# Optimization experiments

Hardware: AMD Instinct MI355X
Metric: run time of the kernel (lower is better)

Reference implementation:

```python
import jax, jax.numpy as jnp
import numpy as np

N_CTX = 4096
D_MODEL = 1024
D_HEAD = 64


def setup_inputs() -> dict:
    key = jax.random.key(0)
    k_x, k_q, k_k, k_o, k_v = jax.random.split(key, 5)
    return {
        "x": jax.random.normal(k_x, (N_CTX, D_MODEL), dtype=jnp.float32),
        "W_q": jax.random.normal(k_q, (D_MODEL, D_HEAD), dtype=jnp.float32),
        "W_kT": jax.random.normal(k_k, (D_HEAD, D_MODEL), dtype=jnp.float32),
        "W_o": jax.random.normal(k_o, (D_MODEL, D_HEAD), dtype=jnp.float32),
        "W_vT": jax.random.normal(k_v, (D_HEAD, D_MODEL), dtype=jnp.float32),
    }


def reference(x, W_q, W_kT, W_o, W_vT):
    # x: [n, d_model]
    n = x.shape[0]
    q = x @ W_q                      # [n, d_head]
    k = x @ W_kT.T                   # [n, d_head]  (W_kT @ x.T transposed)
    scores = q @ k.T                 # [n, n] -- NOTE: original has no 1/sqrt(d_head) scaling
    # causal mask: upper triangle (strictly above diagonal) set to -inf
    causal = jnp.tril(jnp.ones((n, n), dtype=bool))
    scores = jnp.where(causal, scores, -jnp.inf)
    attn = jax.nn.softmax(scores, axis=1)  # softmax over keys (dim=1)
    v = x @ W_o @ W_vT               # [n, d_model] -- faithful to attn @ x @ W_o @ W_vT
    return attn @ v                  # [n, d_model]
```

## Files before the change

### kernel.cpp

```cpp
#include <hip/hip_runtime.h>
#include <hip/hip_bf16.h>
#include <math.h>

#define DM    1024
#define DH    64
#define NCTX  4096
#define NCH   8

typedef __attribute__((ext_vector_type(8))) _Float16 f16x8;
typedef __attribute__((ext_vector_type(4))) float f32x4;

#define D_QH   0
#define D_QM   524288
#define D_KH   1572864
#define D_KM   2097152
#define D_UTB  3145728
#define D_PY   3670016
#define D_PM   12058624
#define D_PL   12189696
#define D_WTH  12320768
#define D_WTM  12713984

#define S_WVH  0
#define S_WVM  131072
#define S_PM   262144
#define S_PL   393216
#define S_PY   524288
#define S_END  8912896
#define S_YH   262144
#define S_YM   786432

__device__ __forceinline__ ushort f2h(float x) {
  _Float16 h = (_Float16)x;
  return __builtin_bit_cast(ushort, h);
}
__device__ __forceinline__ float h2f(ushort u) {
  return (float)__builtin_bit_cast(_Float16, u);
}

typedef __attribute__((address_space(1))) const unsigned int gas_u32;
typedef __attribute__((address_space(3))) unsigned int las_u32;
__device__ __forceinline__ void gload_lds16(const void* g, void* l) {
  __builtin_amdgcn_global_load_lds((gas_u32*)g, (las_u32*)l, 16, 0, 0);
}

__global__ __launch_bounds__(256) void wsplit_kernel(
    const float* __restrict__ Wq, const float* __restrict__ WkT,
    const float* __restrict__ Wo, const float* __restrict__ Wv,
    ushort* __restrict__ WTh, ushort* __restrict__ WTm,
    ushort* __restrict__ WvTh, ushort* __restrict__ WvTm)
{
  int gid = blockIdx.x * 256 + threadIdx.x;
  int mat = gid >> 16;
  int idx = gid & 65535;
  if (mat == 3) {
    float v = Wv[idx];
    int h = idx >> 10, c = idx & 1023;
    int oidx = c * 64 + h;
    ushort h16 = f2h(v);
    WvTh[oidx] = h16;
    WvTm[oidx] = f2h(v - h2f(h16));
    return;
  }
  float v; int oidx;
  if (mat == 1) {
    v = WkT[idx];
    oidx = 65536 + idx;
  } else {
    int k = idx >> 6, h = idx & 63;
    v = (mat == 0 ? Wq : Wo)[idx];
    oidx = mat * 65536 + h * 1024 + k;
  }
  ushort h16 = f2h(v);
  float rem = v - h2f(h16);
  WTh[oidx] = h16;
  WTm[oidx] = f2h(rem);
}

__global__ __launch_bounds__(256, 2) void proj_mfma_kernel(
    const float* __restrict__ x,
    const ushort* __restrict__ WTh, const ushort* __restrict__ WTm,
    ushort* __restrict__ Qh, ushort* __restrict__ Qm,
    ushort* __restrict__ Kh, ushort* __restrict__ Km,
    ushort* __restrict__ UTb)
{
  __shared__ __align__(16) ushort xsh[32*128], xsm[32*128];
  __shared__ __align__(16) ushort wsh[2][64*128], wsm[2][64*128];

  const int tid  = threadIdx.x;
  const int lane = tid & 63;
  const int w    = tid >> 6;
  const int q16  = lane & 15;
  const int grp  = lane >> 4;
  const int r0   = blockIdx.x * 32;
  const int mat  = blockIdx.y;
  const ushort* __restrict__ wh = WTh + mat * 65536;
  const ushort* __restrict__ wm = WTm + mat * 65536;

  const int rw  = (w & 1) * 16;
  const int ct0 = (w >> 1) * 2;

  const int xrowl = tid >> 4, xslot = tid & 15;

  auto stage_w = [&](int b, int s) {
    const int kp0 = s * 128;
    #pragma unroll
    for (int u = 0; u < 4; ++u) {
      int ubase = u * 256 + w * 64;
      int unit  = ubase + lane;
      int row   = unit >> 4, slotp = unit & 15;
      int ssrc  = slotp ^ (row & 15);
      int gsrc  = row * DM + kp0 + ssrc * 8;
      gload_lds16(&wh[gsrc], &wsh[b][ubase * 8]);
      gload_lds16(&wm[gsrc], &wsm[b][ubase * 8]);
    }
  };
  auto xload = [&](int s, float4& a0, float4& a1, float4& b0, float4& b1) {
    const int kp0 = s * 128;
    const float* s0 = &x[(r0 + xrowl) * DM + kp0 + xslot * 8];
    const float* s1 = &x[(r0 + xrowl + 16) * DM + kp0 + xslot * 8];
    a0 = *(const float4*)&s0[0]; a1 = *(const float4*)&s0[4];
    b0 = *(const float4*)&s1[0]; b1 = *(const float4*)&s1[4];
  };
  auto xsplit_write = [&](float4 a0, float4 a1, float4 b0, float4 b1) {
    float xv0[8] = {a0.x,a0.y,a0.z,a0.w,a1.x,a1.y,a1.z,a1.w};
    float xv1[8] = {b0.x,b0.y,b0.z,b0.w,b1.x,b1.y,b1.z,b1.w};
    ushort hv0[8], mv0[8], hv1[8], mv1[8];
    #pragma unroll
    for (int e = 0; e < 8; ++e) {
      ushort h0 = f2h(xv0[e]);
      hv0[e] = h0;  mv0[e] = f2h(xv0[e] - h2f(h0));
      ushort h1 = f2h(xv1[e]);
      hv1[e] = h1;  mv1[e] = f2h(xv1[e] - h2f(h1));
    }
    int d0 = xrowl * 128 + ((xslot ^ (xrowl & 15)) << 3);
    int r1 = xrowl + 16;
    int d1 = r1 * 128 + ((xslot ^ (r1 & 15)) << 3);
    #pragma unroll
    for (int e = 0; e < 8; ++e) {
      xsh[d0+e] = hv0[e]; xsm[d0+e] = mv0[e];
      xsh[d1+e] = hv1[e]; xsm[d1+e] = mv1[e];
    }
  };

  f32x4 acc[2] = {{0,0,0,0},{0,0,0,0}};

  {
    float4 a0, a1, b0, b1;
    xload(0, a0, a1, b0, b1);
    xsplit_write(a0, a1, b0, b1);
    stage_w(0, 0);
  }
  __syncthreads();

  int cur = 0;
  for (int stg = 0; stg < 8; ++stg) {
    float4 na0, na1, nb0, nb1;
    if (stg < 7) {
      xload(stg + 1, na0, na1, nb0, nb1);
      stage_w(cur ^ 1, stg + 1);
    }
    #pragma unroll
    for (int ksub = 0; ksub < 4; ++ksub) {
      const int s = ksub * 4 + grp;
      const int xrow = rw + q16;
      f16x8 xh8 = *(const f16x8*)&xsh[xrow * 128 + ((s ^ (xrow & 15)) << 3)];
      f16x8 xm8 = *(const f16x8*)&xsm[xrow * 128 + ((s ^ (xrow & 15)) << 3)];
      #pragma unroll
      for (int i = 0; i < 2; ++i) {
        const int wrow = (ct0 + i) * 16 + q16;
        const int woff = wrow * 128 + ((s ^ (wrow & 15)) << 3);
        f16x8 bh = *(const f16x8*)&wsh[cur][woff];
        f16x8 bm = *(const f16x8*)&wsm[cur][woff];
        if (mat == 2) {
          acc[i] = __builtin_amdgcn_mfma_f32_16x16x32_f16(bh, xh8, acc[i], 0,0,0);
          acc[i] = __builtin_amdgcn_mfma_f32_16x16x32_f16(bh, xm8, acc[i], 0,0,0);
          acc[i] = __builtin_amdgcn_mfma_f32_16x16x32_f16(bm, xh8, acc[i], 0,0,0);
        } else {
          acc[i] = __builtin_amdgcn_mfma_f32_16x16x32_f16(xh8, bh, acc[i], 0,0,0);
          acc[i] = __builtin_amdgcn_mfma_f32_16x16x32_f16(xh8, bm, acc[i], 0,0,0);
          acc[i] = __builtin_amdgcn_mfma_f32_16x16x32_f16(xm8, bh, acc[i], 0,0,0);
        }
      }
    }
    __syncthreads();
    if (stg < 7) xsplit_write(na0, na1, nb0, nb1);
    __syncthreads();
    cur ^= 1;
  }

  if (mat == 2) {
    #pragma unroll
    for (int i = 0; i < 2; ++i)
      #pragma unroll
      for (int r = 0; r < 4; ++r)
        UTb[((ct0 + i)*16 + 4*grp + r) * NCTX + r0 + rw + q16] = f2h(acc[i][r]);
  } else {
    ushort* __restrict__ Dh = (mat == 0) ? Qh : Kh;
    ushort* __restrict__ Dm = (mat == 0) ? Qm : Km;
    #pragma unroll
    for (int i = 0; i < 2; ++i)
      #pragma unroll
      for (int r = 0; r < 4; ++r) {
        float v = acc[i][r];
        ushort h = f2h(v);
        ushort m = f2h(v - h2f(h));
        int idx = (r0 + rw + 4*grp + r) * DH + (ct0 + i)*16 + q16;
        Dh[idx] = h; Dm[idx] = m;
      }
  }
}

__global__ __launch_bounds__(256, 2) void attn_kernel(
    const ushort* __restrict__ Qh, const ushort* __restrict__ Qm,
    const ushort* __restrict__ Kh, const ushort* __restrict__ Km,
    const ushort* __restrict__ UTb,
    float* __restrict__ Pm, float* __restrict__ Pl, float* __restrict__ Py)
{
  __shared__ ushort Ksh[2][2][64*64];
  __shared__ ushort Ush[2][64*64];
  __shared__ __align__(16) ushort ps[4][16*72];

  const int tid  = threadIdx.x;
  const int lane = tid & 63;
  const int w    = tid >> 6;
  ushort* psw = ps[w];
  const int q16  = lane & 15;
  const int grp  = lane >> 4;
  const int colb = grp * 8;

  const int qq    = blockIdx.x;
  const int c     = blockIdx.y;
  const int gbase = 252 - 4 * qq;
  const int g     = gbase + w;
  const int gmax  = gbase + 3;
  const int T     = ((16*gmax + 15) >> 6) + 1;
  const int t0 = (c * T) >> 3, t1 = ((c+1) * T) >> 3;
  const int Town = ((16*g + 15) >> 6) + 1;
  const int q0 = 16 * g;
  const int q  = q0 + q16;

  auto stage = [&](int b, int t) {
    const int j0 = t * 64;
    #pragma unroll
    for (int it = 0; it < 2; ++it) {
      int ubase = it * 256 + w * 64;
      int unit  = ubase + lane;
      int row   = unit >> 3, slotp = unit & 7;
      int c8    = slotp ^ (row & 7);
      int src   = (j0 + row) * DH + c8 * 8;
      gload_lds16(&Kh[src], &Ksh[b][0][ubase * 8]);
      gload_lds16(&Km[src], &Ksh[b][1][ubase * 8]);
      gload_lds16(&UTb[row * NCTX + j0 + c8 * 8], &Ush[b][ubase * 8]);
    }
  };

  f16x8 fqh[2], fqm[2];
  #pragma unroll
  for (int ks = 0; ks < 2; ++ks) {
    int off = (q0 + q16)*DH + 32*ks + colb;
    fqh[ks] = *(const f16x8*)&Qh[off];
    fqm[ks] = *(const f16x8*)&Qm[off];
  }

  float mrun = -3.0e38f, lrun = 0.f;
  f32x4 yacc[4] = {{0,0,0,0},{0,0,0,0},{0,0,0,0},{0,0,0,0}};

  if (t0 < t1) stage(0, t0);
  __syncthreads();

  int cur = 0;
  for (int t = t0; t < t1; ++t) {
    if (t + 1 < t1) stage(cur ^ 1, t + 1);
    if (t < Town) {
      const int j0 = t * 64;
      f32x4 sa[4] = {{0,0,0,0},{0,0,0,0},{0,0,0,0},{0,0,0,0}};
      #pragma unroll
      for (int ks = 0; ks < 2; ++ks) {
        #pragma unroll
        for (int st = 0; st < 4; ++st) {
          int row = 16*st + q16;
          int off = row * 64 + (((4*ks + grp) ^ (row & 7)) << 3);
          f16x8 kh = *(const f16x8*)&Ksh[cur][0][off];
          f16x8 km = *(const f16x8*)&Ksh[cur][1][off];
          sa[st] = __builtin_amdgcn_mfma_f32_16x16x32_f16(kh, fqh[ks], sa[st], 0,0,0);
          sa[st] = __builtin_amdgcn_mfma_f32_16x16x32_f16(kh, fqm[ks], sa[st], 0,0,0);
          sa[st] = __builtin_amdgcn_mfma_f32_16x16x32_f16(km, fqh[ks], sa[st], 0,0,0);
        }
      }
      #pragma unroll
      for (int st = 0; st < 4; ++st)
        #pragma unroll
        for (int r = 0; r < 4; ++r) {
          int key = j0 + 16*st + 4*grp + r;
          if (key > q) sa[st][r] = -3.0e38f;
        }
      float mx = sa[0][0];
      #pragma unroll
      for (int st = 0; st < 4; ++st)
        #pragma unroll
        for (int r = 0; r < 4; ++r) mx = fmaxf(mx, sa[st][r]);
      mx = fmaxf(mx, __shfl_xor(mx, 16));
      mx = fmaxf(mx, __shfl_xor(mx, 32));
      float mnew  = fmaxf(mrun, mx);
      float alpha = __expf(mrun - mnew);
      float ts = 0.f;
      ushort pb[16];
      #pragma unroll
      for (int st = 0; st < 4; ++st)
        #pragma unroll
        for (int r = 0; r < 4; ++r) {
          float p = __expf(sa[st][r] - mnew);
          ts += p;
          pb[st*4 + r] = f2h(p);
        }
      ts += __shfl_xor(ts, 16);
      ts += __shfl_xor(ts, 32);
      lrun = lrun * alpha + ts;
      mrun = mnew;
      float ar[4];
      #pragma unroll
      for (int r = 0; r < 4; ++r) ar[r] = __shfl(alpha, 4*grp + r, 64);
      #pragma unroll
      for (int dt = 0; dt < 4; ++dt) {
        yacc[dt][0] *= ar[0]; yacc[dt][1] *= ar[1];
        yacc[dt][2] *= ar[2]; yacc[dt][3] *= ar[3];
      }
      #pragma unroll
      for (int st = 0; st < 4; ++st) {
        uint2 v;
        v.x = (uint)pb[st*4+0] | ((uint)pb[st*4+1] << 16);
        v.y = (uint)pb[st*4+2] | ((uint)pb[st*4+3] << 16);
        *(uint2*)&psw[q16*72 + 16*st + 4*grp] = v;
      }
      __threadfence_block();
      __builtin_amdgcn_sched_barrier(0);
      #pragma unroll
      for (int ks = 0; ks < 2; ++ks) {
        f16x8 pa = *(const f16x8*)&psw[q16*72 + 32*ks + colb];
        #pragma unroll
        for (int dt = 0; dt < 4; ++dt) {
          int row = 16*dt + q16;
          int off = row * 64 + (((4*ks + grp) ^ (row & 7)) << 3);
          f16x8 ub = *(const f16x8*)&Ush[cur][off];
          yacc[dt] = __builtin_amdgcn_mfma_f32_16x16x32_f16(pa, ub, yacc[dt], 0,0,0);
        }
      }
    }
    __syncthreads();
    cur ^= 1;
  }
  if (grp == 0) {
    Pm[c * NCTX + q] = mrun;
    Pl[c * NCTX + q] = lrun;
  }
  #pragma unroll
  for (int dt = 0; dt < 4; ++dt)
    #pragma unroll
    for (int r = 0; r < 4; ++r)
      Py[(c * NCTX + q0 + 4*grp + r) * DH + 16*dt + q16] = yacc[dt][r];
}

__global__ __launch_bounds__(256, 3) void out_fused_kernel(
    const float* __restrict__ Pm, const float* __restrict__ Pl,
    const float* __restrict__ Py,
    const ushort* __restrict__ WvTh, const ushort* __restrict__ WvTm,
    float* __restrict__ out)
{
  __shared__ __align__(16) ushort Yh[64*64], Ym[64*64];
  __shared__ __align__(16) ushort Wsh[128*64], Wsm[128*64];
  __shared__ float sden[NCH][64];
  __shared__ float invd[64];

  const int tid  = threadIdx.x;
  const int lane = tid & 63;
  const int w    = tid >> 6;
  const int q16  = lane & 15;
  const int grp  = lane >> 4;
  const int r0   = blockIdx.x * 64;
  const int cb   = blockIdx.y;

  #pragma unroll
  for (int u = 0; u < 4; ++u) {
    int ubase = u * 256 + w * 64;
    int unit  = ubase + lane;
    int row   = unit >> 3, slotp = unit & 7;
    int c8    = slotp ^ (row & 7);
    int src   = (cb * 128 + row) * 64 + c8 * 8;
    gload_lds16(&WvTh[src], &Wsh[ubase * 8]);
    gload_lds16(&WvTm[src], &Wsm[ubase * 8]);
  }
  if (tid < 64) {
    int rrow = r0 + tid;
    float mv[NCH]; float M = -3.0e38f;
    #pragma unroll
    for (int c = 0; c < NCH; ++c) {
      mv[c] = Pm[c*NCTX + rrow];
      M = fmaxf(M, mv[c]);
    }
    float den = 0.f;
    #pragma unroll
    for (int c = 0; c < NCH; ++c) {
      float s = __expf(mv[c] - M);
      sden[c][tid] = s;
      den += s * Pl[c*NCTX + rrow];
    }
    invd[tid] = 1.0f / den;
  }
  __syncthreads();

  #pragma unroll
  for (int it = 0; it < 4; ++it) {
    int idx = it * 256 + tid;
    int h4 = idx & 15, rr = idx >> 4;
    int rrow = r0 + rr;
    float nx = 0.f, ny = 0.f, nz = 0.f, nw = 0.f;
    #pragma unroll
    for (int c = 0; c < NCH; ++c) {
      float s = sden[c][rr];
      float4 p4 = *(const float4*)&Py[(c*NCTX + rrow)*DH + h4*4];
      nx += s*p4.x; ny += s*p4.y; nz += s*p4.z; nw += s*p4.w;
    }
    float inv = invd[rr];
    float yv[4] = {nx*inv, ny*inv, nz*inv, nw*inv};
    ushort hv[4], mv4[4];
    #pragma unroll
    for (int e = 0; e < 4; ++e) {
      ushort h = f2h(yv[e]);
      hv[e] = h;
      mv4[e] = f2h(yv[e] - h2f(h));
    }
    int off = rr*64 + (((h4 >> 1) ^ (rr & 7)) << 3) + (h4 & 1) * 4;
    uint2 vh, vm;
    vh.x = (uint)hv[0] | ((uint)hv[1] << 16);
    vh.y = (uint)hv[2] | ((uint)hv[3] << 16);
    vm.x = (uint)mv4[0] | ((uint)mv4[1] << 16);
    vm.y = (uint)mv4[2] | ((uint)mv4[3] << 16);
    *(uint2*)&Yh[off] = vh;
    *(uint2*)&Ym[off] = vm;
  }
  __syncthreads();

  f32x4 acc[4][2] = {};
  #pragma unroll
  for (int ks = 0; ks < 2; ++ks) {
    f16x8 ah[4], am[4];
    #pragma unroll
    for (int rt = 0; rt < 4; ++rt) {
      int row = 16*rt + q16;
      int off = row*64 + (((4*ks + grp) ^ (row & 7)) << 3);
      ah[rt] = *(const f16x8*)&Yh[off];
      am[rt] = *(const f16x8*)&Ym[off];
    }
    #pragma unroll
    for (int lt = 0; lt < 2; ++lt) {
      int crow = w*32 + lt*16 + q16;
      int off  = crow*64 + (((4*ks + grp) ^ (crow & 7)) << 3);
      f16x8 bh = *(const f16x8*)&Wsh[off];
      f16x8 bm = *(const f16x8*)&Wsm[off];
      #pragma unroll
      for (int rt = 0; rt < 4; ++rt) {
        acc[rt][lt] = __builtin_amdgcn_mfma_f32_16x16x32_f16(ah[rt], bh, acc[rt][lt], 0,0,0);
        acc[rt][lt] = __builtin_amdgcn_mfma_f32_16x16x32_f16(ah[rt], bm, acc[rt][lt], 0,0,0);
        acc[rt][lt] = __builtin_amdgcn_mfma_f32_16x16x32_f16(am[rt], bh, acc[rt][lt], 0,0,0);
      }
    }
  }
  #pragma unroll
  for (int rt = 0; rt < 4; ++rt)
    #pragma unroll
    for (int lt = 0; lt < 2; ++lt)
      #pragma unroll
      for (int r = 0; r < 4; ++r)
        out[(r0 + 16*rt + 4*grp + r) * DM + cb*128 + w*32 + lt*16 + q16] = acc[rt][lt][r];
}

__global__ __launch_bounds__(256) void combine_kernel(
    const float* __restrict__ Pm, const float* __restrict__ Pl,
    const float* __restrict__ Py,
    ushort* __restrict__ Yh, ushort* __restrict__ Ym)
{
  int idx = blockIdx.x * 256 + threadIdx.x;
  int r = idx >> 6, d = idx & 63;
  float mv[NCH];
  float M = -3.0e38f;
  #pragma unroll
  for (int c = 0; c < NCH; ++c) {
    mv[c] = Pm[c*NCTX + r];
    M = fmaxf(M, mv[c]);
  }
  float num = 0.f, den = 0.f;
  #pragma unroll
  for (int c = 0; c < NCH; ++c) {
    float s = __expf(mv[c] - M);
    den += s * Pl[c*NCTX + r];
    num += s * Py[(c*NCTX + r)*DH + d];
  }
  float y = num / den;
  ushort h = f2h(y);
  Yh[idx] = h;
  Ym[idx] = f2h(y - h2f(h));
}

__global__ __launch_bounds__(256, 3) void out_mfma_kernel(
    const ushort* __restrict__ Yh_g, const ushort* __restrict__ Ym_g,
    const ushort* __restrict__ WvTh, const ushort* __restrict__ WvTm,
    float* __restrict__ out)
{
  __shared__ __align__(16) ushort Yh[64*64], Ym[64*64];
  __shared__ __align__(16) ushort Wsh[128*64], Wsm[128*64];

  const int tid  = threadIdx.x;
  const int lane = tid & 63;
  const int w    = tid >> 6;
  const int q16  = lane & 15;
  const int grp  = lane >> 4;
  const int r0   = blockIdx.x * 64;
  const int cb   = blockIdx.y;

  #pragma unroll
  for (int it = 0; it < 2; ++it) {
    int ubase = it * 256 + w * 64;
    int unit  = ubase + lane;
    int row   = unit >> 3, slotp = unit & 7;
    int c8    = slotp ^ (row & 7);
    int src   = (r0 + row) * 64 + c8 * 8;
    gload_lds16(&Yh_g[src], &Yh[ubase * 8]);
    gload_lds16(&Ym_g[src], &Ym[ubase * 8]);
  }
  #pragma unroll
  for (int u = 0; u < 4; ++u) {
    int ubase = u * 256 + w * 64;
    int unit  = ubase + lane;
    int row   = unit >> 3, slotp = unit & 7;
    int c8    = slotp ^ (row & 7);
    int src   = (cb * 128 + row) * 64 + c8 * 8;
    gload_lds16(&WvTh[src], &Wsh[ubase * 8]);
    gload_lds16(&WvTm[src], &Wsm[ubase * 8]);
  }
  __syncthreads();

  f32x4 acc[4][2] = {};
  #pragma unroll
  for (int ks = 0; ks < 2; ++ks) {
    f16x8 ah[4], am[4];
    #pragma unroll
    for (int rt = 0; rt < 4; ++rt) {
      int row = 16*rt + q16;
      int off = row*64 + (((4*ks + grp) ^ (row & 7)) << 3);
      ah[rt] = *(const f16x8*)&Yh[off];
      am[rt] = *(const f16x8*)&Ym[off];
    }
    #pragma unroll
    for (int lt = 0; lt < 2; ++lt) {
      int crow = w*32 + lt*16 + q16;
      int off  = crow*64 + (((4*ks + grp) ^ (crow & 7)) << 3);
      f16x8 bh = *(const f16x8*)&Wsh[off];
      f16x8 bm = *(const f16x8*)&Wsm[off];
      #pragma unroll
      for (int rt = 0; rt < 4; ++rt) {
        acc[rt][lt] = __builtin_amdgcn_mfma_f32_16x16x32_f16(ah[rt], bh, acc[rt][lt], 0,0,0);
        acc[rt][lt] = __builtin_amdgcn_mfma_f32_16x16x32_f16(ah[rt], bm, acc[rt][lt], 0,0,0);
        acc[rt][lt] = __builtin_amdgcn_mfma_f32_16x16x32_f16(am[rt], bh, acc[rt][lt], 0,0,0);
      }
    }
  }
  #pragma unroll
  for (int rt = 0; rt < 4; ++rt)
    #pragma unroll
    for (int lt = 0; lt < 2; ++lt)
      #pragma unroll
      for (int r = 0; r < 4; ++r)
        out[(r0 + 16*rt + 4*grp + r) * DM + cb*128 + w*32 + lt*16 + q16] = acc[rt][lt][r];
}

extern "C" void kernel_launch(void* const* d_in, const int* in_sizes, int n_in,
                              void* d_out, int out_size, void* d_ws, size_t ws_size,
                              hipStream_t stream) {
  const float* x   = (const float*)d_in[0];
  const float* Wq  = (const float*)d_in[1];
  const float* WkT = (const float*)d_in[2];
  const float* Wo  = (const float*)d_in[3];
  const float* Wv  = (const float*)d_in[4];
  float* out = (float*)d_out;
  char*  ob  = (char*)d_out;
  char*  wb  = (char*)d_ws;

  ushort* Qhp = (ushort*)(ob + D_QH);
  ushort* Qmp = (ushort*)(ob + D_QM);
  ushort* Khp = (ushort*)(ob + D_KH);
  ushort* Kmp = (ushort*)(ob + D_KM);
  ushort* UTb = (ushort*)(ob + D_UTB);
  ushort* WTh = (ushort*)(ob + D_WTH);
  ushort* WTm = (ushort*)(ob + D_WTM);

  ushort* WvTh = (ushort*)(wb + S_WVH);
  ushort* WvTm = (ushort*)(wb + S_WVM);

  const bool big_ws = (ws_size >= (size_t)S_END);

  float* Pmp = big_ws ? (float*)(wb + S_PM) : (float*)(ob + D_PM);
  float* Plp = big_ws ? (float*)(wb + S_PL) : (float*)(ob + D_PL);
  float* Pyp = big_ws ? (float*)(wb + S_PY) : (float*)(ob + D_PY);

  hipLaunchKernelGGL(wsplit_kernel, dim3(1024), dim3(256), 0, stream,
                     Wq, WkT, Wo, Wv, WTh, WTm, WvTh, WvTm);
  hipLaunchKernelGGL(proj_mfma_kernel, dim3(128, 3), dim3(256), 0, stream,
                     x, WTh, WTm, Qhp, Qmp, Khp, Kmp, UTb);
  hipLaunchKernelGGL(attn_kernel, dim3(64, 8), dim3(256), 0, stream,
                     Qhp, Qmp, Khp, Kmp, UTb, Pmp, Plp, Pyp);
  if (big_ws) {
    hipLaunchKernelGGL(out_fused_kernel, dim3(64, 8), dim3(256), 0, stream,
                       Pmp, Plp, Pyp, WvTh, WvTm, out);
  } else {
    ushort* Yhp = (ushort*)(wb + S_YH);
    ushort* Ymp = (ushort*)(wb + S_YM);
    hipLaunchKernelGGL(combine_kernel, dim3(1024), dim3(256), 0, stream,
                       Pmp, Plp, Pyp, Yhp, Ymp);
    hipLaunchKernelGGL(out_mfma_kernel, dim3(64, 8), dim3(256), 0, stream,
                       Yhp, Ymp, WvTh, WvTm, out);
  }
}
```

Measured before the change: 55.08 us.

## Fuse split-KV combine and output projection into attention via last-block counter

The separate out_fused kernel is removed. Its combine-and-project epilogue now runs inside attn_kernel: an atomic counter per query tile elects the last of the 8 KV-chunk blocks, which merges the partial softmax states and multiplies by W_vT across all 8 column blocks. This also moves intermediates into the workspace under a larger workspace threshold, and adds a memset to clear the counters. The intent is to save a kernel launch and its tail. The cost is that one block per query tile serially does eight output tiles' worth of work, which can lengthen the critical path. It also relies on the workspace being large enough for the new layout, and otherwise falls back to the old multi-kernel path.

```diff
diff --git a/kernel.cpp b/kernel.cpp
--- a/kernel.cpp
+++ b/kernel.cpp
@@ -9,6 +9,21 @@
 
 typedef __attribute__((ext_vector_type(8))) _Float16 f16x8;
 typedef __attribute__((ext_vector_type(4))) float f32x4;
+
+#define P_WVH  0
+#define P_WVM  131072
+#define P_CNT  262144
+#define P_WTH  266240
+#define P_WTM  659456
+#define P_QH   1052672
+#define P_QM   1576960
+#define P_KH   2101248
+#define P_KM   2625536
+#define P_UTB  3149824
+#define P_PM   3674112
+#define P_PL   3805184
+#define P_PY   3936256
+#define P_END  12324864
 
 #define D_QH   0
 #define D_QM   524288
@@ -20,13 +35,8 @@
 #define D_PL   12189696
 #define D_WTH  12320768
 #define D_WTM  12713984
-
 #define S_WVH  0
 #define S_WVM  131072
-#define S_PM   262144
-#define S_PL   393216
-#define S_PY   524288
-#define S_END  8912896
 #define S_YH   262144
 #define S_YM   786432
 
@@ -211,20 +221,35 @@
   }
 }
 
+union SmemU {
+  struct {
+    ushort Ksh[2][2][64*64];
+    ushort Ush[2][64*64];
+    ushort ps[4][16*72];
+  } a;
+  struct {
+    ushort Yh[64*64], Ym[64*64];
+    ushort Wsh[128*64], Wsm[128*64];
+    float  sden[NCH][64];
+    float  invd[64];
+  } f;
+};
+
 __global__ __launch_bounds__(256, 2) void attn_kernel(
     const ushort* __restrict__ Qh, const ushort* __restrict__ Qm,
     const ushort* __restrict__ Kh, const ushort* __restrict__ Km,
     const ushort* __restrict__ UTb,
-    float* __restrict__ Pm, float* __restrict__ Pl, float* __restrict__ Py)
+    float* __restrict__ Pm, float* __restrict__ Pl, float* __restrict__ Py,
+    const ushort* __restrict__ WvTh, const ushort* __restrict__ WvTm,
+    float* __restrict__ out, int* __restrict__ cnt, int do_fin)
 {
-  __shared__ ushort Ksh[2][2][64*64];
-  __shared__ ushort Ush[2][64*64];
-  __shared__ __align__(16) ushort ps[4][16*72];
+  __shared__ __align__(16) SmemU sm;
+  __shared__ int fin;
 
   const int tid  = threadIdx.x;
   const int lane = tid & 63;
   const int w    = tid >> 6;
-  ushort* psw = ps[w];
+  ushort* psw = sm.a.ps[w];
   const int q16  = lane & 15;
   const int grp  = lane >> 4;
   const int colb = grp * 8;
@@ -249,9 +274,9 @@
       int row   = unit >> 3, slotp = unit & 7;
       int c8    = slotp ^ (row & 7);
       int src   = (j0 + row) * DH + c8 * 8;
-      gload_lds16(&Kh[src], &Ksh[b][0][ubase * 8]);
-      gload_lds16(&Km[src], &Ksh[b][1][ubase * 8]);
-      gload_lds16(&UTb[row * NCTX + j0 + c8 * 8], &Ush[b][ubase * 8]);
+      gload_lds16(&Kh[src], &sm.a.Ksh[b][0][ubase * 8]);
+      gload_lds16(&Km[src], &sm.a.Ksh[b][1][ubase * 8]);
+      gload_lds16(&UTb[row * NCTX + j0 + c8 * 8], &sm.a.Ush[b][ubase * 8]);
     }
   };
 
@@ -281,8 +306,8 @@
         for (int st = 0; st < 4; ++st) {
           int row = 16*st + q16;
           int off = row * 64 + (((4*ks + grp) ^ (row & 7)) << 3);
-          f16x8 kh = *(const f16x8*)&Ksh[cur][0][off];
-          f16x8 km = *(const f16x8*)&Ksh[cur][1][off];
+          f16x8 kh = *(const f16x8*)&sm.a.Ksh[cur][0][off];
+          f16x8 km = *(const f16x8*)&sm.a.Ksh[cur][1][off];
           sa[st] = __builtin_amdgcn_mfma_f32_16x16x32_f16(kh, fqh[ks], sa[st], 0,0,0);
           sa[st] = __builtin_amdgcn_mfma_f32_16x16x32_f16(kh, fqm[ks], sa[st], 0,0,0);
           sa[st] = __builtin_amdgcn_mfma_f32_16x16x32_f16(km, fqh[ks], sa[st], 0,0,0);
@@ -342,7 +367,7 @@
         for (int dt = 0; dt < 4; ++dt) {
           int row = 16*dt + q16;
           int off = row * 64 + (((4*ks + grp) ^ (row & 7)) << 3);
-          f16x8 ub = *(const f16x8*)&Ush[cur][off];
+          f16x8 ub = *(const f16x8*)&sm.a.Ush[cur][off];
           yacc[dt] = __builtin_amdgcn_mfma_f32_16x16x32_f16(pa, ub, yacc[dt], 0,0,0);
         }
       }
@@ -359,53 +384,37 @@
     #pragma unroll
     for (int r = 0; r < 4; ++r)
       Py[(c * NCTX + q0 + 4*grp + r) * DH + 16*dt + q16] = yacc[dt][r];
-}
-
-__global__ __launch_bounds__(256, 3) void out_fused_kernel(
-    const float* __restrict__ Pm, const float* __restrict__ Pl,
-    const float* __restrict__ Py,
-    const ushort* __restrict__ WvTh, const ushort* __restrict__ WvTm,
-    float* __restrict__ out)
-{
-  __shared__ __align__(16) ushort Yh[64*64], Ym[64*64];
-  __shared__ __align__(16) ushort Wsh[128*64], Wsm[128*64];
-  __shared__ float sden[NCH][64];
-  __shared__ float invd[64];
-
-  const int tid  = threadIdx.x;
-  const int lane = tid & 63;
-  const int w    = tid >> 6;
-  const int q16  = lane & 15;
-  const int grp  = lane >> 4;
-  const int r0   = blockIdx.x * 64;
-  const int cb   = blockIdx.y;
-
-  #pragma unroll
-  for (int u = 0; u < 4; ++u) {
-    int ubase = u * 256 + w * 64;
-    int unit  = ubase + lane;
-    int row   = unit >> 3, slotp = unit & 7;
-    int c8    = slotp ^ (row & 7);
-    int src   = (cb * 128 + row) * 64 + c8 * 8;
-    gload_lds16(&WvTh[src], &Wsh[ubase * 8]);
-    gload_lds16(&WvTm[src], &Wsm[ubase * 8]);
-  }
+
+  if (!do_fin) return;
+
+  __threadfence();
+  __syncthreads();
+  if (tid == 0) {
+    int old = atomicAdd(&cnt[qq], 1);
+    fin = (old == 7);
+  }
+  __syncthreads();
+  if (!fin) return;
+  __threadfence();
+
+  const int rq0 = 16 * gbase;
+
   if (tid < 64) {
-    int rrow = r0 + tid;
+    int rrow = rq0 + tid;
     float mv[NCH]; float M = -3.0e38f;
     #pragma unroll
-    for (int c = 0; c < NCH; ++c) {
-      mv[c] = Pm[c*NCTX + rrow];
-      M = fmaxf(M, mv[c]);
+    for (int cc = 0; cc < NCH; ++cc) {
+      mv[cc] = Pm[cc*NCTX + rrow];
+      M = fmaxf(M, mv[cc]);
     }
     float den = 0.f;
     #pragma unroll
-    for (int c = 0; c < NCH; ++c) {
-      float s = __expf(mv[c] - M);
-      sden[c][tid] = s;
-      den += s * Pl[c*NCTX + rrow];
-    }
-    invd[tid] = 1.0f / den;
+    for (int cc = 0; cc < NCH; ++cc) {
+      float s = __expf(mv[cc] - M);
+      sm.f.sden[cc][tid] = s;
+      den += s * Pl[cc*NCTX + rrow];
+    }
+    sm.f.invd[tid] = 1.0f / den;
   }
   __syncthreads();
 
@@ -413,15 +422,15 @@
   for (int it = 0; it < 4; ++it) {
     int idx = it * 256 + tid;
     int h4 = idx & 15, rr = idx >> 4;
-    int rrow = r0 + rr;
+    int rrow = rq0 + rr;
     float nx = 0.f, ny = 0.f, nz = 0.f, nw = 0.f;
     #pragma unroll
-    for (int c = 0; c < NCH; ++c) {
-      float s = sden[c][rr];
-      float4 p4 = *(const float4*)&Py[(c*NCTX + rrow)*DH + h4*4];
+    for (int cc = 0; cc < NCH; ++cc) {
+      float s = sm.f.sden[cc][rr];
+      float4 p4 = *(const float4*)&Py[(cc*NCTX + rrow)*DH + h4*4];
       nx += s*p4.x; ny += s*p4.y; nz += s*p4.z; nw += s*p4.w;
     }
-    float inv = invd[rr];
+    float inv = sm.f.invd[rr];
     float yv[4] = {nx*inv, ny*inv, nz*inv, nw*inv};
     ushort hv[4], mv4[4];
     #pragma unroll
@@ -436,43 +445,57 @@
     vh.y = (uint)hv[2] | ((uint)hv[3] << 16);
     vm.x = (uint)mv4[0] | ((uint)mv4[1] << 16);
     vm.y = (uint)mv4[2] | ((uint)mv4[3] << 16);
-    *(uint2*)&Yh[off] = vh;
-    *(uint2*)&Ym[off] = vm;
-  }
-  __syncthreads();
-
-  f32x4 acc[4][2] = {};
-  #pragma unroll
-  for (int ks = 0; ks < 2; ++ks) {
-    f16x8 ah[4], am[4];
-    #pragma unroll
-    for (int rt = 0; rt < 4; ++rt) {
-      int row = 16*rt + q16;
-      int off = row*64 + (((4*ks + grp) ^ (row & 7)) << 3);
-      ah[rt] = *(const f16x8*)&Yh[off];
-      am[rt] = *(const f16x8*)&Ym[off];
-    }
-    #pragma unroll
-    for (int lt = 0; lt < 2; ++lt) {
-      int crow = w*32 + lt*16 + q16;
-      int off  = crow*64 + (((4*ks + grp) ^ (crow & 7)) << 3);
-      f16x8 bh = *(const f16x8*)&Wsh[off];
-      f16x8 bm = *(const f16x8*)&Wsm[off];
+    *(uint2*)&sm.f.Yh[off] = vh;
+    *(uint2*)&sm.f.Ym[off] = vm;
+  }
+
+  for (int cb2 = 0; cb2 < 8; ++cb2) {
+    __syncthreads();
+    #pragma unroll
+    for (int u = 0; u < 4; ++u) {
+      int ubase = u * 256 + w * 64;
+      int unit  = ubase + lane;
+      int row   = unit >> 3, slotp = unit & 7;
+      int c8    = slotp ^ (row & 7);
+      int src   = (cb2 * 128 + row) * 64 + c8 * 8;
+      gload_lds16(&WvTh[src], &sm.f.Wsh[ubase * 8]);
+      gload_lds16(&WvTm[src], &sm.f.Wsm[ubase * 8]);
+    }
+    __syncthreads();
+
+    f32x4 acc[4][2] = {};
+    #pragma unroll
+    for (int ks = 0; ks < 2; ++ks) {
+      f16x8 ah[4], am[4];
       #pragma unroll
       for (int rt = 0; rt < 4; ++rt) {
-        acc[rt][lt] = __builtin_amdgcn_mfma_f32_16x16x32_f16(ah[rt], bh, acc[rt][lt], 0,0,0);
-        acc[rt][lt] = __builtin_amdgcn_mfma_f32_16x16x32_f16(ah[rt], bm, acc[rt][lt], 0,0,0);
-        acc[rt][lt] = __builtin_amdgcn_mfma_f32_16x16x32_f16(am[rt], bh, acc[rt][lt], 0,0,0);
-      }
-    }
-  }
-  #pragma unroll
-  for (int rt = 0; rt < 4; ++rt)
-    #pragma unroll
-    for (int lt = 0; lt < 2; ++lt)
-      #pragma unroll
-      for (int r = 0; r < 4; ++r)
-        out[(r0 + 16*rt + 4*grp + r) * DM + cb*128 + w*32 + lt*16 + q16] = acc[rt][lt][r];
+        int row = 16*rt + q16;
+        int off = row*64 + (((4*ks + grp) ^ (row & 7)) << 3);
+        ah[rt] = *(const f16x8*)&sm.f.Yh[off];
+        am[rt] = *(const f16x8*)&sm.f.Ym[off];
+      }
+      #pragma unroll
+      for (int lt = 0; lt < 2; ++lt) {
+        int crow = w*32 + lt*16 + q16;
+        int off  = crow*64 + (((4*ks + grp) ^ (crow & 7)) << 3);
+        f16x8 bh = *(const f16x8*)&sm.f.Wsh[off];
+        f16x8 bm = *(const f16x8*)&sm.f.Wsm[off];
+        #pragma unroll
+        for (int rt = 0; rt < 4; ++rt) {
+          acc[rt][lt] = __builtin_amdgcn_mfma_f32_16x16x32_f16(ah[rt], bh, acc[rt][lt], 0,0,0);
+          acc[rt][lt] = __builtin_amdgcn_mfma_f32_16x16x32_f16(ah[rt], bm, acc[rt][lt], 0,0,0);
+          acc[rt][lt] = __builtin_amdgcn_mfma_f32_16x16x32_f16(am[rt], bh, acc[rt][lt], 0,0,0);
+        }
+      }
+    }
+    #pragma unroll
+    for (int rt = 0; rt < 4; ++rt)
+      #pragma unroll
+      for (int lt = 0; lt < 2; ++lt)
+        #pragma unroll
+        for (int r = 0; r < 4; ++r)
+          out[(rq0 + 16*rt + 4*grp + r) * DM + cb2*128 + w*32 + lt*16 + q16] = acc[rt][lt][r];
+  }
 }
 
 __global__ __launch_bounds__(256) void combine_kernel(
@@ -586,35 +609,54 @@
   char*  ob  = (char*)d_out;
   char*  wb  = (char*)d_ws;
 
-  ushort* Qhp = (ushort*)(ob + D_QH);
-  ushort* Qmp = (ushort*)(ob + D_QM);
-  ushort* Khp = (ushort*)(ob + D_KH);
-  ushort* Kmp = (ushort*)(ob + D_KM);
-  ushort* UTb = (ushort*)(ob + D_UTB);
-  ushort* WTh = (ushort*)(ob + D_WTH);
-  ushort* WTm = (ushort*)(ob + D_WTM);
-
-  ushort* WvTh = (ushort*)(wb + S_WVH);
-  ushort* WvTm = (ushort*)(wb + S_WVM);
-
-  const bool big_ws = (ws_size >= (size_t)S_END);
-
-  float* Pmp = big_ws ? (float*)(wb + S_PM) : (float*)(ob + D_PM);
-  float* Plp = big_ws ? (float*)(wb + S_PL) : (float*)(ob + D_PL);
-  float* Pyp = big_ws ? (float*)(wb + S_PY) : (float*)(ob + D_PY);
-
-  hipLaunchKernelGGL(wsplit_kernel, dim3(1024), dim3(256), 0, stream,
-                     Wq, WkT, Wo, Wv, WTh, WTm, WvTh, WvTm);
-  hipLaunchKernelGGL(proj_mfma_kernel, dim3(128, 3), dim3(256), 0, stream,
-                     x, WTh, WTm, Qhp, Qmp, Khp, Kmp, UTb);
-  hipLaunchKernelGGL(attn_kernel, dim3(64, 8), dim3(256), 0, stream,
-                     Qhp, Qmp, Khp, Kmp, UTb, Pmp, Plp, Pyp);
+  const bool big_ws = (ws_size >= (size_t)P_END);
+
   if (big_ws) {
-    hipLaunchKernelGGL(out_fused_kernel, dim3(64, 8), dim3(256), 0, stream,
-                       Pmp, Plp, Pyp, WvTh, WvTm, out);
+    ushort* WvTh = (ushort*)(wb + P_WVH);
+    ushort* WvTm = (ushort*)(wb + P_WVM);
+    int*    cnt  = (int*)(wb + P_CNT);
+    ushort* WTh  = (ushort*)(wb + P_WTH);
+    ushort* WTm  = (ushort*)(wb + P_WTM);
+    ushort* Qhp  = (ushort*)(wb + P_QH);
+    ushort* Qmp  = (ushort*)(wb + P_QM);
+    ushort* Khp  = (ushort*)(wb + P_KH);
+    ushort* Kmp  = (ushort*)(wb + P_KM);
+    ushort* UTb  = (ushort*)(wb + P_UTB);
+    float*  Pmp  = (float*)(wb + P_PM);
+    float*  Plp  = (float*)(wb + P_PL);
+    float*  Pyp  = (float*)(wb + P_PY);
+
+    hipMemsetAsync(cnt, 0, 256, stream);
+    hipLaunchKernelGGL(wsplit_kernel, dim3(1024), dim3(256), 0, stream,
+                       Wq, WkT, Wo, Wv, WTh, WTm, WvTh, WvTm);
+    hipLaunchKernelGGL(proj_mfma_kernel, dim3(128, 3), dim3(256), 0, stream,
+                       x, WTh, WTm, Qhp, Qmp, Khp, Kmp, UTb);
+    hipLaunchKernelGGL(attn_kernel, dim3(64, 8), dim3(256), 0, stream,
+                       Qhp, Qmp, Khp, Kmp, UTb, Pmp, Plp, Pyp,
+                       WvTh, WvTm, out, cnt, 1);
   } else {
-    ushort* Yhp = (ushort*)(wb + S_YH);
-    ushort* Ymp = (ushort*)(wb + S_YM);
+    ushort* Qhp = (ushort*)(ob + D_QH);
+    ushort* Qmp = (ushort*)(ob + D_QM);
+    ushort* Khp = (ushort*)(ob + D_KH);
+    ushort* Kmp = (ushort*)(ob + D_KM);
+    ushort* UTb = (ushort*)(ob + D_UTB);
+    ushort* WTh = (ushort*)(ob + D_WTH);
+    ushort* WTm = (ushort*)(ob + D_WTM);
+    float*  Pmp = (float*)(ob + D_PM);
+    float*  Plp = (float*)(ob + D_PL);
+    float*  Pyp = (float*)(ob + D_PY);
+    ushort* WvTh = (ushort*)(wb + S_WVH);
+    ushort* WvTm = (ushort*)(wb + S_WVM);
+    ushort* Yhp  = (ushort*)(wb + S_YH);
+    ushort* Ymp  = (ushort*)(wb + S_YM);
+
+    hipLaunchKernelGGL(wsplit_kernel, dim3(1024), dim3(256), 0, stream,
+                       Wq, WkT, Wo, Wv, WTh, WTm, WvTh, WvTm);
+    hipLaunchKernelGGL(proj_mfma_kernel, dim3(128, 3), dim3(256), 0, stream,
+                       x, WTh, WTm, Qhp, Qmp, Khp, Kmp, UTb);
+    hipLaunchKernelGGL(attn_kernel, dim3(64, 8), dim3(256), 0, stream,
+                       Qhp, Qmp, Khp, Kmp, UTb, Pmp, Plp, Pyp,
+                       WvTh, WvTm, out, (int*)nullptr, 0);
     hipLaunchKernelGGL(combine_kernel, dim3(1024), dim3(256), 0, stream,
                        Pmp, Plp, Pyp, Yhp, Ymp);
     hipLaunchKernelGGL(out_mfma_kernel, dim3(64, 8), dim3(256), 0, stream,
```

New measurement: 125.3 us. 2.27x slower.
